# Kernel tuning notes

Hardware: AMD Instinct MI355X
Metric: run time of the kernel (lower is better)

Reference implementation:

```python
import jax, jax.numpy as jnp
import numpy as np

B, N, H, V, MAX_STEPS = 16, 512, 256, 32000, 48


def setup_inputs() -> dict:
    key = jax.random.key(0)
    ks = jax.random.split(key, 10)
    sH = 1.0 / np.sqrt(H)
    s2H = 1.0 / np.sqrt(2 * H)
    return {
        'node_embeddings': jax.random.normal(ks[0], (B, N, H), dtype=jnp.float32),
        'Wx': jax.random.normal(ks[1], (H, 4 * H), dtype=jnp.float32) * sH,
        'Wh': jax.random.normal(ks[2], (H, 4 * H), dtype=jnp.float32) * sH,
        'b': jnp.zeros((4 * H,), jnp.float32),
        'Wb': jax.random.normal(ks[3], (2 * H, 2), dtype=jnp.float32) * s2H,
        'bb': jnp.zeros((2,), jnp.float32),
        'Wo': jax.random.normal(ks[4], (2 * H, V), dtype=jnp.float32) * s2H,
        'bo': jnp.zeros((V,), jnp.float32),
        'true_indexes': jax.random.randint(ks[5], (B, N), 0, N, dtype=jnp.int32),
        'false_indexes': jax.random.randint(ks[6], (B, N), 0, N, dtype=jnp.int32),
        'exit_indexes': jax.random.randint(ks[7], (B,), 0, N, dtype=jnp.int32),
        'steps': jax.random.randint(ks[8], (B,), 1, MAX_STEPS, dtype=jnp.int32),
    }


def reference(node_embeddings, Wx, Wh, b, Wb, bb, Wo, bo,
              true_indexes, false_indexes, exit_indexes, steps):
    num_nodes = node_embeddings.shape[1]
    hidden = Wx.shape[0]

    def single_example(node_emb, t_idx, f_idx, exit_i, n_steps):
        c0 = jnp.zeros((num_nodes, hidden), node_emb.dtype)
        h0 = jnp.zeros((num_nodes, hidden), node_emb.dtype)
        ip0 = jnp.zeros((num_nodes,), node_emb.dtype).at[0].set(1.0)

        def seg(x, idx):
            return jax.ops.segment_sum(x, idx, num_segments=num_nodes)

        def step(carry, _):
            c, h, ip, idx = carry
            # LSTM cell vmapped over nodes (gate order i,f,g,o)
            z = node_emb @ Wx + h @ Wh + b  # [N, 4H]
            i, f, g, o = jnp.split(z, 4, axis=-1)
            c2 = jax.nn.sigmoid(f) * c + jax.nn.sigmoid(i) * jnp.tanh(g)
            h2 = jax.nn.sigmoid(o) * jnp.tanh(c2)
            # exit node keeps its previous hidden state
            c2 = c2.at[exit_i].set(c[exit_i])
            h2 = h2.at[exit_i].set(h[exit_i])
            # branch decision on concat(c, h)
            hcat = jnp.concatenate([c2, h2], axis=-1)  # [N, 2H]
            bd = jax.nn.softmax(hcat @ Wb + bb, axis=-1)
            pt = bd[:, 0] * ip  # [N]
            pf = bd[:, 1] * ip
            ip_new = seg(pt, t_idx) + seg(pf, f_idx)
            denom = (ip_new + 1e-7)[:, None]
            c_new = (seg(c2 * pt[:, None], t_idx) + seg(c2 * pf[:, None], f_idx)) / denom
            h_new = (seg(h2 * pt[:, None], t_idx) + seg(h2 * pf[:, None], f_idx)) / denom
            keep = idx < n_steps
            carry = (jnp.where(keep, c_new, c), jnp.where(keep, h_new, h),
                     jnp.where(keep, ip_new, ip), idx + 1)
            return carry, None

        (c, h, _, _), _ = jax.lax.scan(step, (c0, h0, ip0, jnp.int32(0)), None, length=MAX_STEPS)
        final = jnp.concatenate([c[exit_i], h[exit_i]], axis=-1)  # [2H]
        return final @ Wo + bo  # [V]

    logits = jax.vmap(single_example)(node_embeddings, true_indexes, false_indexes,
                                      exit_indexes, steps)
    return logits[:, None, :]  # [B, 1, V]
```

## Files before the change

kernel.cpp:

```cpp
#include <hip/hip_runtime.h>
#include <hip/hip_bf16.h>

constexpr int kB  = 16;
constexpr int kN  = 512;
constexpr int kH  = 256;
constexpr int kH4 = 1024;
constexpr int kV  = 32000;
constexpr int kS  = 48;

typedef __attribute__((ext_vector_type(8))) short short8v;
typedef __attribute__((ext_vector_type(4))) float f32x4;
typedef unsigned short u16;

__device__ __forceinline__ float sigm(float x){ return 1.f/(1.f+expf(-x)); }
__device__ __forceinline__ float fsigm(float x){
  return __builtin_amdgcn_rcpf(1.f + __expf(-x));
}
__device__ __forceinline__ float ftanh(float x){
  return 1.f - 2.f*__builtin_amdgcn_rcpf(1.f + __expf(2.f*x));
}

__device__ __forceinline__ u16 f2bf(float f){
  __hip_bfloat16 h = __float2bfloat16(f);
  return __builtin_bit_cast(u16, h);
}
__device__ __forceinline__ float bf2f(u16 u){
  __hip_bfloat16 h = __builtin_bit_cast(__hip_bfloat16, u);
  return __bfloat162float(h);
}

__global__ void k_csr(const int* t_idx, const int* f_idx, int* offsets, int* entries){
  int b = blockIdx.x; int t = threadIdx.x;
  __shared__ int tl[kN], fl[kN], cnt[kN], pos[kN], ebuf[2*kN];
  tl[t] = t_idx[b*kN+t]; fl[t] = f_idx[b*kN+t];
  cnt[t] = 0;
  __syncthreads();
  atomicAdd(&cnt[tl[t]], 1);
  atomicAdd(&cnt[fl[t]], 1);
  __syncthreads();
  int myc = cnt[t];
  pos[t] = myc;
  __syncthreads();
  for (int off=1; off<kN; off<<=1){
    int v = pos[t];
    int add = (t>=off)? pos[t-off] : 0;
    __syncthreads();
    pos[t] = v + add;
    __syncthreads();
  }
  int excl = pos[t] - myc;
  offsets[b*(kN+1)+t] = excl;
  if (t==0) offsets[b*(kN+1)+kN] = 2*kN;
  __syncthreads();
  pos[t] = excl;
  __syncthreads();
  int p1 = atomicAdd(&pos[tl[t]], 1); ebuf[p1] = t;
  int p2 = atomicAdd(&pos[fl[t]], 1); ebuf[p2] = t | (1<<16);
  __syncthreads();
  for (int i = excl+1; i < excl+myc; ++i){
    int v = ebuf[i]; int j = i-1;
    while (j >= excl && ebuf[j] > v){ ebuf[j+1] = ebuf[j]; --j; }
    ebuf[j+1] = v;
  }
  __syncthreads();
  entries[b*2*kN + t]      = ebuf[t];
  entries[b*2*kN + kN + t] = ebuf[kN + t];
}

__global__ void k_pack2(const float* __restrict__ Wh, const float* __restrict__ Wx,
                        u16* __restrict__ Whh, u16* __restrict__ Wxh){
  int id = blockIdx.x; int l = threadIdx.x;
  bool isWh = (id < 512);
  const float* W = isWh ? Wh : Wx;
  u16* ph = isWh ? Whh : Wxh;
  int fi = id & 511;
  int kt = fi >> 6; int wo = (fi>>4)&3; int cfl = fi & 15;
  int g = cfl>>2; int j = cfl&3;
  int col = g*kH + wo*64 + j*16 + (l&15);
  int kb = kt*32 + (l>>4)*8;
  size_t o = (size_t)fi*512 + (size_t)l*8;
  #pragma unroll
  for (int jj=0; jj<8; ++jj){
    float w = W[(size_t)(kb+jj)*kH4 + col];
    ph[o+jj] = f2bf(w);
  }
}

__global__ __launch_bounds__(1024) void k_x_mfma(
    const float* __restrict__ emb,
    const u16* __restrict__ Wxp_hi,
    const float* __restrict__ bias, u16* __restrict__ Xp)
{
  int blk = blockIdx.x;
  int b = blk >> 4; int row0 = (blk & 15) * 32;
  int tid = threadIdx.x;
  int wn = tid >> 6, lane = tid & 63;
  int lrow = lane & 15, lk = lane >> 4;
  int ch = wn*16 + lrow;

  f32x4 acc[2][4];
  #pragma unroll
  for (int r=0;r<2;r++)
    #pragma unroll
    for (int g=0;g<4;g++){
      float bv = bias[g*kH + ch];
      acc[r][g] = (f32x4){bv,bv,bv,bv};
    }

  const float* eb_ = emb + ((size_t)b*kN + row0)*kH;
  int wo = wn >> 2, jj4 = wn & 3;
  for (int kt=0; kt<8; ++kt){
    short8v a_hi[2], a_lo[2];
    #pragma unroll
    for (int r=0;r<2;r++){
      size_t off = (size_t)(r*16+lrow)*kH + kt*32 + lk*8;
      float4 v0 = *(const float4*)(eb_ + off);
      float4 v1 = *(const float4*)(eb_ + off + 4);
      float vv[8] = {v0.x,v0.y,v0.z,v0.w,v1.x,v1.y,v1.z,v1.w};
      #pragma unroll
      for (int q=0;q<8;q++){
        u16 hi = f2bf(vv[q]);
        a_hi[r][q] = (short)hi;
        a_lo[r][q] = (short)f2bf(vv[q] - bf2f(hi));
      }
    }
    #pragma unroll
    for (int g=0; g<4; ++g){
      size_t fb = ((size_t)((kt*4+wo)*16 + g*4 + jj4))*512 + (size_t)lane*8;
      short8v bh = *(const short8v*)(Wxp_hi+fb);
      #pragma unroll
      for (int r=0;r<2;r++){
        acc[r][g] = __builtin_amdgcn_mfma_f32_16x16x32_bf16(a_hi[r], bh, acc[r][g], 0,0,0);
        acc[r][g] = __builtin_amdgcn_mfma_f32_16x16x32_bf16(a_lo[r], bh, acc[r][g], 0,0,0);
      }
    }
  }

  ushort4* xb = (ushort4*)(Xp + ((size_t)blk*16 + wn)*2048);
  #pragma unroll
  for (int r=0;r<2;r++)
    #pragma unroll
    for (int g=0;g<4;g++){
      ushort4 xv;
      xv.x = f2bf(acc[r][g][0]); xv.y = f2bf(acc[r][g][1]);
      xv.z = f2bf(acc[r][g][2]); xv.w = f2bf(acc[r][g][3]);
      xb[(r*4+g)*64 + lane] = xv;
    }
}

__global__ __launch_bounds__(1024) void k_fused(
    const u16* __restrict__ Xp,
    const u16* __restrict__ Wp_hi,
    const float* __restrict__ Wb, const float* __restrict__ bb,
    const int* __restrict__ exit_idx, const int* __restrict__ steps,
    const int* __restrict__ offsets, const int* __restrict__ entries,
    const float* __restrict__ c2r, const u16* __restrict__ h2r,
    const float* __restrict__ ptr_, const float* __restrict__ pfr,
    float* __restrict__ c2w, u16* __restrict__ h2w,
    float* __restrict__ ptw, float* __restrict__ pfw,
    float* __restrict__ exf, int s)
{
  int blk = blockIdx.x;
  int b = blk >> 4;
  int st = steps[b];
  if (s > st) return;
  int row0 = (blk & 15) * 32;
  int tid = threadIdx.x;
  int wn = tid >> 6, lane = tid & 63;
  int lrow = lane & 15, lk = lane >> 4;
  int ch = wn*16 + lrow;
  int eb = exit_idx[b];
  int wo = wn >> 2, jj4 = wn & 3;
  bool fin = (s == st);

  __shared__ u16 hh_lds[32*256];
  __shared__ float c_lds[32][260];
  __shared__ float ip_lds[32];
  __shared__ float prs[16][32][2];

  f32x4 acc[2][4];
  if (!fin){
    const ushort4* xb = (const ushort4*)(Xp + ((size_t)blk*16 + wn)*2048);
    #pragma unroll
    for (int r=0;r<2;r++)
      #pragma unroll
      for (int g=0;g<4;g++){
        ushort4 xv = xb[(r*4+g)*64 + lane];
        acc[r][g] = (f32x4){bf2f(xv.x), bf2f(xv.y), bf2f(xv.z), bf2f(xv.w)};
      }
  }

  if (s == 0){
    for (int i = tid; i < 32*256; i += 1024) hh_lds[i] = 0;
    for (int i = tid; i < 32*260; i += 1024) (&c_lds[0][0])[i] = 0.f;
    if (tid < 32) ip_lds[tid] = (row0 + tid == 0) ? 1.f : 0.f;
  } else {
    const float* c2rb = c2r + (size_t)b*kN*kH;
    const u16*   h2rb = h2r + (size_t)b*kN*kH;
    const int*   ebL  = entries + b*2*kN;
    const int*   offB = offsets + b*(kN+1);
    const float* ptb_ = ptr_ + b*kN;
    const float* pfb_ = pfr  + b*kN;
    #pragma unroll
    for (int mi = 0; mi < 2; ++mi){
      int mloc = wn*2 + mi;
      int m = row0 + mloc;
      if (fin && m != eb) continue;
      int start = offB[m], end = offB[m+1];
      float4 aC = {0.f,0.f,0.f,0.f}, aH = {0.f,0.f,0.f,0.f};
      float aP = 0.f;
      for (int e = start; e < end; e += 4){
        int   se[4]; float pv[4];
        #pragma unroll
        for (int q=0;q<4;q++){
          bool ok = (e+q < end);
          int ent = ebL[ok ? e+q : e];
          int src = ent & 0xFFFF;
          float p = (ent>>16) ? pfb_[src] : ptb_[src];
          se[q] = src;
          pv[q] = ok ? p : 0.f;
        }
        float4 cv[4]; ushort4 hv[4];
        #pragma unroll
        for (int q=0;q<4;q++){
          cv[q] = *(const float4*)&c2rb[(size_t)se[q]*kH + lane*4];
          hv[q] = *(const ushort4*)&h2rb[(size_t)se[q]*kH + lane*4];
        }
        #pragma unroll
        for (int q=0;q<4;q++){
          aP += pv[q];
          aC.x += pv[q]*cv[q].x; aC.y += pv[q]*cv[q].y;
          aC.z += pv[q]*cv[q].z; aC.w += pv[q]*cv[q].w;
          aH.x += pv[q]*bf2f(hv[q].x); aH.y += pv[q]*bf2f(hv[q].y);
          aH.z += pv[q]*bf2f(hv[q].z); aH.w += pv[q]*bf2f(hv[q].w);
        }
      }
      float inv = 1.f/(aP + 1e-7f);
      float oc[4] = {aC.x*inv, aC.y*inv, aC.z*inv, aC.w*inv};
      float oh[4] = {aH.x*inv, aH.y*inv, aH.z*inv, aH.w*inv};
      if (fin){
        *(float4*)&exf[b*2*kH + lane*4]      = *(float4*)oc;
        *(float4*)&exf[b*2*kH + kH + lane*4] = *(float4*)oh;
      } else {
        *(float4*)&c_lds[mloc][lane*4] = *(float4*)oc;
        ushort4 hh4;
        u16* hhp = (u16*)&hh4;
        #pragma unroll
        for (int q=0;q<4;q++) hhp[q] = f2bf(oh[q]);
        int bo2 = (mloc*512 + lane*8) ^ ((mloc&7)<<4);
        *(ushort4*)((char*)hh_lds + bo2) = hh4;
        if (lane == 0) ip_lds[mloc] = aP;
      }
    }
  }
  if (fin) return;
  __syncthreads();

  if (s > 0){
    for (int kt=0; kt<8; ++kt){
      short8v a[2];
      #pragma unroll
      for (int r=0;r<2;r++){
        int row = r*16 + lrow;
        int bo2 = (row*512 + kt*64 + lk*16) ^ ((row&7)<<4);
        a[r] = *(const short8v*)((char*)hh_lds + bo2);
      }
      #pragma unroll
      for (int g=0; g<4; ++g){
        size_t fb = ((size_t)((kt*4+wo)*16 + g*4 + jj4))*512 + (size_t)lane*8;
        short8v bh = *(const short8v*)(Wp_hi+fb);
        #pragma unroll
        for (int r=0;r<2;r++)
          acc[r][g] = __builtin_amdgcn_mfma_f32_16x16x32_bf16(a[r], bh, acc[r][g], 0,0,0);
      }
    }
  }

  float wbc0 = Wb[ch*2+0],      wbc1 = Wb[ch*2+1];
  float wbh0 = Wb[(kH+ch)*2+0], wbh1 = Wb[(kH+ch)*2+1];
  float pr0[8], pr1[8];
  #pragma unroll
  for (int r=0;r<2;r++)
    #pragma unroll
    for (int reg=0;reg<4;reg++){
      int rloc = r*16 + lk*4 + reg;
      int row = row0 + rloc;
      float zi = acc[r][0][reg];
      float zf = acc[r][1][reg];
      float zg = acc[r][2][reg];
      float zo = acc[r][3][reg];
      float cp = c_lds[rloc][ch];
      float c2v = fsigm(zf)*cp + fsigm(zi)*ftanh(zg);
      float h2v = fsigm(zo)*ftanh(c2v);
      if (row == eb){
        int bo2 = (rloc*512 + ch*2) ^ ((rloc&7)<<4);
        c2v = cp;
        h2v = bf2f(*(const u16*)((const char*)hh_lds + bo2));
      }
      size_t gb = ((size_t)b*kN + row)*kH + ch;
      c2w[gb] = c2v;
      h2w[gb] = f2bf(h2v);
      int pi = r*4+reg;
      pr0[pi] = c2v*wbc0 + h2v*wbh0;
      pr1[pi] = c2v*wbc1 + h2v*wbh1;
    }

  #pragma unroll
  for (int off=1; off<16; off<<=1){
    #pragma unroll
    for (int i=0;i<8;i++){
      pr0[i] += __shfl_xor(pr0[i], off);
      pr1[i] += __shfl_xor(pr1[i], off);
    }
  }
  if (lrow == 0){
    #pragma unroll
    for (int r=0;r<2;r++)
      #pragma unroll
      for (int reg=0;reg<4;reg++){
        int lr = r*16 + lk*4 + reg;
        prs[wn][lr][0] = pr0[r*4+reg];
        prs[wn][lr][1] = pr1[r*4+reg];
      }
  }
  __syncthreads();
  if (tid < 32){
    int row = row0 + tid;
    float u0 = bb[0], u1 = bb[1];
    #pragma unroll
    for (int w=0;w<16;w++){ u0 += prs[w][tid][0]; u1 += prs[w][tid][1]; }
    float mx = fmaxf(u0,u1);
    float e0 = expf(u0-mx), e1 = expf(u1-mx);
    float inv = 1.f/(e0+e1);
    float ipv = ip_lds[tid];
    ptw[b*kN+row] = (e0*inv)*ipv;
    pfw[b*kN+row] = (e1*inv)*ipv;
  }
}

__global__ __launch_bounds__(256) void k_out_part(
    const float* __restrict__ exf, const float* __restrict__ Wo,
    float* __restrict__ partial)
{
  int kq = blockIdx.x / 125;
  int vt = blockIdx.x % 125;
  int t = threadIdx.x;
  __shared__ float sf[kB][128];
  for (int i = t; i < kB*128; i += 256){
    int b = i >> 7; int kl = i & 127;
    sf[b][kl] = exf[b*2*kH + kq*128 + kl];
  }
  __syncthreads();
  int v = vt*256 + t;
  float acc[kB];
  #pragma unroll
  for (int b=0;b<kB;b++) acc[b] = 0.f;
  int k0 = kq*128;
  for (int kl=0; kl<128; kl+=4){
    float w0 = Wo[(size_t)(k0+kl+0)*kV + v];
    float w1 = Wo[(size_t)(k0+kl+1)*kV + v];
    float w2 = Wo[(size_t)(k0+kl+2)*kV + v];
    float w3 = Wo[(size_t)(k0+kl+3)*kV + v];
    #pragma unroll
    for (int b=0;b<kB;b++){
      float4 s4 = *(const float4*)&sf[b][kl];
      acc[b] += s4.x*w0 + s4.y*w1 + s4.z*w2 + s4.w*w3;
    }
  }
  #pragma unroll
  for (int b=0;b<kB;b++) partial[(size_t)(kq*kB+b)*kV + v] = acc[b];
}

__global__ __launch_bounds__(256) void k_out_sum(
    const float* __restrict__ partial, const float* __restrict__ bo,
    float* __restrict__ out)
{
  int v = blockIdx.x*256 + threadIdx.x;
  if (v >= kV) return;
  float bv = bo[v];
  #pragma unroll
  for (int b=0;b<kB;b++){
    float s = bv;
    #pragma unroll
    for (int q=0;q<4;q++) s += partial[(size_t)(q*kB+b)*kV + v];
    out[(size_t)b*kV + v] = s;
  }
}

extern "C" void kernel_launch(void* const* d_in, const int* in_sizes, int n_in,
                              void* d_out, int out_size, void* d_ws, size_t ws_size,
                              hipStream_t stream) {
  const float* emb   = (const float*)d_in[0];
  const float* Wx    = (const float*)d_in[1];
  const float* Wh    = (const float*)d_in[2];
  const float* bias  = (const float*)d_in[3];
  const float* Wb    = (const float*)d_in[4];
  const float* bbias = (const float*)d_in[5];
  const float* Wo    = (const float*)d_in[6];
  const float* bo    = (const float*)d_in[7];
  const int* t_idx   = (const int*)d_in[8];
  const int* f_idx   = (const int*)d_in[9];
  const int* exit_i  = (const int*)d_in[10];
  const int* steps   = (const int*)d_in[11];
  float* out = (float*)d_out;

  char* ws = (char*)d_ws;
  u16* Xp  = (u16*)ws;    ws += (size_t)kB*kN*kH4*2;
  float* c2a = (float*)ws; ws += (size_t)kB*kN*kH*4;
  float* c2b = (float*)ws; ws += (size_t)kB*kN*kH*4;
  u16* h2a = (u16*)ws;    ws += (size_t)kB*kN*kH*2;
  u16* h2b = (u16*)ws;    ws += (size_t)kB*kN*kH*2;
  u16* Wp_hi  = (u16*)ws; ws += (size_t)kH*kH4*2;
  u16* Wxp_hi = (u16*)ws; ws += (size_t)kH*kH4*2;
  float* pta = (float*)ws; ws += (size_t)kB*kN*4;
  float* pfa = (float*)ws; ws += (size_t)kB*kN*4;
  float* ptb = (float*)ws; ws += (size_t)kB*kN*4;
  float* pfb = (float*)ws; ws += (size_t)kB*kN*4;
  float* exf = (float*)ws; ws += (size_t)kB*2*kH*4;
  int* offsets = (int*)ws; ws += ((size_t)kB*(kN+1)*4 + 255) & ~(size_t)255;
  int* entries = (int*)ws; ws += (size_t)kB*2*kN*4;
  float* partial = (float*)ws; ws += (size_t)4*kB*kV*4;

  k_csr<<<kB, kN, 0, stream>>>(t_idx, f_idx, offsets, entries);
  k_pack2<<<1024, 64, 0, stream>>>(Wh, Wx, Wp_hi, Wxp_hi);
  k_x_mfma<<<256, 1024, 0, stream>>>(emb, Wxp_hi, bias, Xp);

  for (int s = 0; s < kS; ++s){
    bool even = ((s & 1) == 0);
    k_fused<<<256, 1024, 0, stream>>>(
        Xp, Wp_hi, Wb, bbias, exit_i, steps, offsets, entries,
        even ? c2b : c2a, even ? h2b : h2a, even ? ptb : pta, even ? pfb : pfa,
        even ? c2a : c2b, even ? h2a : h2b, even ? pta : ptb, even ? pfa : pfb,
        exf, s);
  }

  k_out_part<<<500, 256, 0, stream>>>(exf, Wo, partial);
  k_out_sum<<<125, 256, 0, stream>>>(partial, bo, out);
}
```

Before: 821.2 us.

## Merge prep kernels, interleave batch across blocks, prefetch Wh fragments

Merges the CSR build and weight packing into a single prep launch, which removes one kernel launch. Blocks are remapped so the batch index is the low bits of the block id, interleaving examples across the grid. This is meant to spread early-exiting examples (fewer steps) more evenly over CUs. The recurrent MFMA loop now software-pipelines the Wh fragment loads, fetching the next k-tile's B operands while the current tile computes, at the cost of extra registers.

```diff
diff --git a/kernel.cpp b/kernel.cpp
--- a/kernel.cpp
+++ b/kernel.cpp
@@ -29,60 +29,64 @@
   return __bfloat162float(h);
 }
 
-__global__ void k_csr(const int* t_idx, const int* f_idx, int* offsets, int* entries){
-  int b = blockIdx.x; int t = threadIdx.x;
+__global__ __launch_bounds__(512) void k_prep(
+    const int* t_idx, const int* f_idx, int* offsets, int* entries,
+    const float* __restrict__ Wh, const float* __restrict__ Wx,
+    u16* __restrict__ Whh, u16* __restrict__ Wxh)
+{
   __shared__ int tl[kN], fl[kN], cnt[kN], pos[kN], ebuf[2*kN];
-  tl[t] = t_idx[b*kN+t]; fl[t] = f_idx[b*kN+t];
-  cnt[t] = 0;
-  __syncthreads();
-  atomicAdd(&cnt[tl[t]], 1);
-  atomicAdd(&cnt[fl[t]], 1);
-  __syncthreads();
-  int myc = cnt[t];
-  pos[t] = myc;
-  __syncthreads();
-  for (int off=1; off<kN; off<<=1){
-    int v = pos[t];
-    int add = (t>=off)? pos[t-off] : 0;
-    __syncthreads();
-    pos[t] = v + add;
-    __syncthreads();
-  }
-  int excl = pos[t] - myc;
-  offsets[b*(kN+1)+t] = excl;
-  if (t==0) offsets[b*(kN+1)+kN] = 2*kN;
-  __syncthreads();
-  pos[t] = excl;
-  __syncthreads();
-  int p1 = atomicAdd(&pos[tl[t]], 1); ebuf[p1] = t;
-  int p2 = atomicAdd(&pos[fl[t]], 1); ebuf[p2] = t | (1<<16);
-  __syncthreads();
-  for (int i = excl+1; i < excl+myc; ++i){
-    int v = ebuf[i]; int j = i-1;
-    while (j >= excl && ebuf[j] > v){ ebuf[j+1] = ebuf[j]; --j; }
-    ebuf[j+1] = v;
-  }
-  __syncthreads();
-  entries[b*2*kN + t]      = ebuf[t];
-  entries[b*2*kN + kN + t] = ebuf[kN + t];
-}
-
-__global__ void k_pack2(const float* __restrict__ Wh, const float* __restrict__ Wx,
-                        u16* __restrict__ Whh, u16* __restrict__ Wxh){
-  int id = blockIdx.x; int l = threadIdx.x;
-  bool isWh = (id < 512);
-  const float* W = isWh ? Wh : Wx;
-  u16* ph = isWh ? Whh : Wxh;
-  int fi = id & 511;
-  int kt = fi >> 6; int wo = (fi>>4)&3; int cfl = fi & 15;
-  int g = cfl>>2; int j = cfl&3;
-  int col = g*kH + wo*64 + j*16 + (l&15);
-  int kb = kt*32 + (l>>4)*8;
-  size_t o = (size_t)fi*512 + (size_t)l*8;
-  #pragma unroll
-  for (int jj=0; jj<8; ++jj){
-    float w = W[(size_t)(kb+jj)*kH4 + col];
-    ph[o+jj] = f2bf(w);
+  if (blockIdx.x < kB){
+    int b = blockIdx.x; int t = threadIdx.x;
+    tl[t] = t_idx[b*kN+t]; fl[t] = f_idx[b*kN+t];
+    cnt[t] = 0;
+    __syncthreads();
+    atomicAdd(&cnt[tl[t]], 1);
+    atomicAdd(&cnt[fl[t]], 1);
+    __syncthreads();
+    int myc = cnt[t];
+    pos[t] = myc;
+    __syncthreads();
+    for (int off=1; off<kN; off<<=1){
+      int v = pos[t];
+      int add = (t>=off)? pos[t-off] : 0;
+      __syncthreads();
+      pos[t] = v + add;
+      __syncthreads();
+    }
+    int excl = pos[t] - myc;
+    offsets[b*(kN+1)+t] = excl;
+    if (t==0) offsets[b*(kN+1)+kN] = 2*kN;
+    __syncthreads();
+    pos[t] = excl;
+    __syncthreads();
+    int p1 = atomicAdd(&pos[tl[t]], 1); ebuf[p1] = t;
+    int p2 = atomicAdd(&pos[fl[t]], 1); ebuf[p2] = t | (1<<16);
+    __syncthreads();
+    for (int i = excl+1; i < excl+myc; ++i){
+      int v = ebuf[i]; int j = i-1;
+      while (j >= excl && ebuf[j] > v){ ebuf[j+1] = ebuf[j]; --j; }
+      ebuf[j+1] = v;
+    }
+    __syncthreads();
+    entries[b*2*kN + t]      = ebuf[t];
+    entries[b*2*kN + kN + t] = ebuf[kN + t];
+  } else {
+    int task = (blockIdx.x - kB)*512 + threadIdx.x;
+    int id = task >> 6; int l = task & 63;
+    bool isWh = (id < 512);
+    const float* W = isWh ? Wh : Wx;
+    u16* ph = isWh ? Whh : Wxh;
+    int fi = id & 511;
+    int kt = fi >> 6; int wo = (fi>>4)&3; int cfl = fi & 15;
+    int g = cfl>>2; int j = cfl&3;
+    int col = g*kH + wo*64 + j*16 + (l&15);
+    int kb = kt*32 + (l>>4)*8;
+    size_t o = (size_t)fi*512 + (size_t)l*8;
+    #pragma unroll
+    for (int jj=0; jj<8; ++jj){
+      float w = W[(size_t)(kb+jj)*kH4 + col];
+      ph[o+jj] = f2bf(w);
+    }
   }
 }
 
@@ -92,7 +96,7 @@
     const float* __restrict__ bias, u16* __restrict__ Xp)
 {
   int blk = blockIdx.x;
-  int b = blk >> 4; int row0 = (blk & 15) * 32;
+  int b = blk & 15; int row0 = (blk >> 4) * 32;
   int tid = threadIdx.x;
   int wn = tid >> 6, lane = tid & 63;
   int lrow = lane & 15, lk = lane >> 4;
@@ -161,10 +165,10 @@
     float* __restrict__ exf, int s)
 {
   int blk = blockIdx.x;
-  int b = blk >> 4;
+  int b = blk & 15;
   int st = steps[b];
   if (s > st) return;
-  int row0 = (blk & 15) * 32;
+  int row0 = (blk >> 4) * 32;
   int tid = threadIdx.x;
   int wn = tid >> 6, lane = tid & 63;
   int lrow = lane & 15, lk = lane >> 4;
@@ -178,7 +182,10 @@
   __shared__ float ip_lds[32];
   __shared__ float prs[16][32][2];
 
+  const u16* bp = Wp_hi + (size_t)wo*8192 + (size_t)jj4*512 + (size_t)lane*8;
+
   f32x4 acc[2][4];
+  short8v bcur[4];
   if (!fin){
     const ushort4* xb = (const ushort4*)(Xp + ((size_t)blk*16 + wn)*2048);
     #pragma unroll
@@ -188,6 +195,10 @@
         ushort4 xv = xb[(r*4+g)*64 + lane];
         acc[r][g] = (f32x4){bf2f(xv.x), bf2f(xv.y), bf2f(xv.z), bf2f(xv.w)};
       }
+    if (s > 0){
+      #pragma unroll
+      for (int g=0;g<4;g++) bcur[g] = *(const short8v*)(bp + g*2048);
+    }
   }
 
   if (s == 0){
@@ -257,6 +268,7 @@
   __syncthreads();
 
   if (s > 0){
+    #pragma unroll
     for (int kt=0; kt<8; ++kt){
       short8v a[2];
       #pragma unroll
@@ -265,14 +277,19 @@
         int bo2 = (row*512 + kt*64 + lk*16) ^ ((row&7)<<4);
         a[r] = *(const short8v*)((char*)hh_lds + bo2);
       }
-      #pragma unroll
-      for (int g=0; g<4; ++g){
-        size_t fb = ((size_t)((kt*4+wo)*16 + g*4 + jj4))*512 + (size_t)lane*8;
-        short8v bh = *(const short8v*)(Wp_hi+fb);
+      short8v bnxt[4];
+      {
+        int kto = (kt < 7) ? (kt+1)*32768 : 7*32768;
+        #pragma unroll
+        for (int g=0;g<4;g++) bnxt[g] = *(const short8v*)(bp + kto + g*2048);
+      }
+      #pragma unroll
+      for (int g=0; g<4; ++g)
         #pragma unroll
         for (int r=0;r<2;r++)
-          acc[r][g] = __builtin_amdgcn_mfma_f32_16x16x32_bf16(a[r], bh, acc[r][g], 0,0,0);
-      }
+          acc[r][g] = __builtin_amdgcn_mfma_f32_16x16x32_bf16(a[r], bcur[g], acc[r][g], 0,0,0);
+      #pragma unroll
+      for (int g=0;g<4;g++) bcur[g] = bnxt[g];
     }
   }
 
@@ -421,8 +438,7 @@
   int* entries = (int*)ws; ws += (size_t)kB*2*kN*4;
   float* partial = (float*)ws; ws += (size_t)4*kB*kV*4;
 
-  k_csr<<<kB, kN, 0, stream>>>(t_idx, f_idx, offsets, entries);
-  k_pack2<<<1024, 64, 0, stream>>>(Wh, Wx, Wp_hi, Wxp_hi);
+  k_prep<<<144, 512, 0, stream>>>(t_idx, f_idx, offsets, entries, Wh, Wx, Wp_hi, Wxp_hi);
   k_x_mfma<<<256, 1024, 0, stream>>>(emb, Wxp_hi, bias, Xp);
 
   for (int s = 0; s < kS; ++s){
```

New measurement: 776.6 us. -5.4%, faster.
